# Kernel optimization log

Hardware: AMD Instinct MI355X
Metric: run time of the kernel (lower is better)

The kernel has to match this reference:

```python
import jax, jax.numpy as jnp
import numpy as np

N_NODES = 50000
N_EDGES = 600000
N_FEAT = 64
D = 128
N_GRAPHS = 1024
N_LAYERS = 4


def setup_inputs() -> dict:
    key = jax.random.key(0)
    ks = jax.random.split(key, 16)
    x = jax.random.normal(ks[0], (N_NODES, N_FEAT), dtype=jnp.float32)
    edge_index = jax.random.randint(ks[1], (2, N_EDGES), 0, N_NODES, dtype=jnp.int64)
    batch_index = jnp.sort(jax.random.randint(ks[2], (N_NODES,), 0, N_GRAPHS, dtype=jnp.int64))
    def lin(k, fan_in, fan_out):
        s = 1.0 / np.sqrt(fan_in)
        kw, kb = jax.random.split(k)
        w = jax.random.uniform(kw, (fan_in, fan_out), minval=-s, maxval=s, dtype=jnp.float32)
        b = jax.random.uniform(kb, (fan_out,), minval=-s, maxval=s, dtype=jnp.float32)
        return w, b
    w0, b0 = lin(ks[3], N_FEAT, D)
    w1, b1 = lin(ks[4], D, D)
    w2, b2 = lin(ks[5], D, D)
    w3, b3 = lin(ks[6], D, D)
    wp, bp = lin(ks[7], D, D)
    return {"x": x, "edge_index": edge_index, "batch_index": batch_index,
            "w0": w0, "b0": b0, "w1": w1, "b1": b1, "w2": w2, "b2": b2,
            "w3": w3, "b3": b3, "wp": wp, "bp": bp}


def _gin_layer(x, src, dst, w, b):
    # GINConv with eps=0: MLP(x_i + sum_{j in N(i)} x_j); MLP = Linear -> ReLU
    agg = jax.ops.segment_sum(x[src], dst, num_segments=N_NODES)
    return jax.nn.relu((x + agg) @ w + b)


def reference(x, edge_index, batch_index, w0, b0, w1, b1, w2, b2, w3, b3, wp, bp):
    src, dst = edge_index[0], edge_index[1]
    # first layer changes width 64 -> 128; agg happens in input width
    agg0 = jax.ops.segment_sum(x[src], dst, num_segments=N_NODES)
    h = jax.nn.relu((x + agg0) @ w0 + b0)
    for w, b in ((w1, b1), (w2, b2), (w3, b3)):
        h = _gin_layer(h, src, dst, w, b)
    # global mean pool per graph
    sums = jax.ops.segment_sum(h, batch_index, num_segments=N_GRAPHS)
    counts = jax.ops.segment_sum(jnp.ones((N_NODES,), dtype=h.dtype), batch_index, num_segments=N_GRAPHS)
    pooled = sums / jnp.maximum(counts, 1.0)[:, None]
    # post_mp: Linear -> ReLU (dropout identity at inference)
    return jax.nn.relu(pooled @ wp + bp)
```

## Files before the change

### kernel.cpp

```cpp
#include <hip/hip_runtime.h>
#include <hip/hip_fp16.h>


#define N_NODES  50000
#define N_EDGES  600000
#define N_FEAT   64
#define DIM      128
#define N_GRAPHS 1024
#define NC       7
#define CSH      13
#define TOT2     (N_NODES * NC)
#define SCH      2048
#define NBLK     ((TOT2 + SCH - 1) / SCH)
#define TPB      256
#define GT32     ((N_NODES + 31) / 32)

typedef _Float16 f16x8 __attribute__((ext_vector_type(8)));
typedef float    f32x4 __attribute__((ext_vector_type(4)));

#define CNTZ2 (TOT2 / 4)
#define XWORK (N_NODES * N_FEAT / 4)
#define CONV_TOTAL (XWORK + N_FEAT * DIM + 3 * DIM * DIM)
#define FILL_TOTAL (N_EDGES + CONV_TOTAL)

__global__ __launch_bounds__(TPB) void zero_k(int* __restrict__ cnt2) {
  int i = blockIdx.x * TPB + threadIdx.x;
  if (i < CNTZ2)
    *reinterpret_cast<int4*>(cnt2 + i * 4) = make_int4(0, 0, 0, 0);
}

__global__ __launch_bounds__(TPB) void hist_k(
    const int* __restrict__ src, const int* __restrict__ dst,
    int* __restrict__ cnt2, int* __restrict__ rank) {
  int e = blockIdx.x * TPB + threadIdx.x;
  if (e >= N_EDGES) return;
  int key = dst[e] * NC + (src[e] >> CSH);
  rank[e] = atomicAdd(&cnt2[key], 1);
}

__global__ __launch_bounds__(TPB) void scan_part_k(
    const int* __restrict__ cnt2, int* __restrict__ part) {
  __shared__ int ws[4];
  int t = threadIdx.x, b = blockIdx.x;
  int base = b * SCH + t * 8;
  int s = 0;
  if (base < TOT2) {
    int4 a = *reinterpret_cast<const int4*>(cnt2 + base);
    int4 c = *reinterpret_cast<const int4*>(cnt2 + base + 4);
    s = a.x + a.y + a.z + a.w + c.x + c.y + c.z + c.w;
  }
  for (int off = 32; off; off >>= 1) s += __shfl_down(s, off, 64);
  int lane = t & 63, wv = t >> 6;
  if (lane == 0) ws[wv] = s;
  __syncthreads();
  if (t == 0) part[b] = ws[0] + ws[1] + ws[2] + ws[3];
}

__global__ __launch_bounds__(TPB) void scan_write_k(
    const int* __restrict__ cnt2, const int* __restrict__ part,
    int* __restrict__ row_ptr2) {
  __shared__ int pscan[TPB];
  __shared__ int wsum[4];
  int t = threadIdx.x, b = blockIdx.x;
  int lane = t & 63, wv = t >> 6;
  int base = b * SCH + t * 8;

  pscan[t] = (t < NBLK) ? part[t] : 0;
  __syncthreads();
  for (int off = 1; off < TPB; off <<= 1) {
    int v = (t >= off) ? pscan[t - off] : 0;
    __syncthreads();
    pscan[t] += v;
    __syncthreads();
  }
  int blk_off = (b > 0) ? pscan[b - 1] : 0;

  int v[8] = {0,0,0,0,0,0,0,0};
  if (base < TOT2) {
    int4 a = *reinterpret_cast<const int4*>(cnt2 + base);
    int4 c = *reinterpret_cast<const int4*>(cnt2 + base + 4);
    v[0]=a.x; v[1]=a.y; v[2]=a.z; v[3]=a.w;
    v[4]=c.x; v[5]=c.y; v[6]=c.z; v[7]=c.w;
  }
  int ls = 0;
#pragma unroll
  for (int i = 0; i < 8; ++i) ls += v[i];
  int incl = ls;
  for (int off = 1; off < 64; off <<= 1) {
    int u = __shfl_up(incl, off, 64);
    if (lane >= off) incl += u;
  }
  if (lane == 63) wsum[wv] = incl;
  __syncthreads();
  int woff = 0;
  for (int w = 0; w < wv; ++w) woff += wsum[w];
  int run = blk_off + woff + (incl - ls);
  if (base < TOT2) {
    int rp[8];
#pragma unroll
    for (int i = 0; i < 8; ++i) { rp[i] = run; run += v[i]; }
    *reinterpret_cast<int4*>(row_ptr2 + base) = make_int4(rp[0], rp[1], rp[2], rp[3]);
    *reinterpret_cast<int4*>(row_ptr2 + base + 4) = make_int4(rp[4], rp[5], rp[6], rp[7]);
  }
  if (b == 0 && t == 0) row_ptr2[TOT2] = N_EDGES;
}

__global__ __launch_bounds__(TPB) void fill_k(
    const int* __restrict__ src, const int* __restrict__ dst,
    const int* __restrict__ row_ptr2, const int* __restrict__ rank,
    int* __restrict__ csr_src,
    const float* __restrict__ x, __half* __restrict__ xh,
    const float* __restrict__ w0, const float* __restrict__ w1,
    const float* __restrict__ w2, const float* __restrict__ w3,
    __half* __restrict__ Wt0, __half* __restrict__ Wt1,
    __half* __restrict__ Wt2, __half* __restrict__ Wt3) {
  int i = blockIdx.x * TPB + threadIdx.x;
  if (i < N_EDGES) {
    int s = src[i];
    int key = dst[i] * NC + (s >> CSH);
    csr_src[row_ptr2[key] + rank[i]] = s;
    return;
  }
  i -= N_EDGES;
  if (i < XWORK) {
    float4 v = *reinterpret_cast<const float4*>(x + (size_t)i * 4);
    union { __half2 h2[2]; uint2 u; } pk;
    pk.h2[0] = __floats2half2_rn(v.x, v.y);
    pk.h2[1] = __floats2half2_rn(v.z, v.w);
    *reinterpret_cast<uint2*>(xh + (size_t)i * 4) = pk.u;
    return;
  }
  int j = i - XWORK;
  if (j < N_FEAT * DIM) {
    int k = j >> 7, n = j & 127;
    Wt0[n * N_FEAT + k] = __float2half(w0[j]);
    return;
  }
  j -= N_FEAT * DIM;
  if (j >= 3 * DIM * DIM) return;
  int wsel = j / (DIM * DIM);
  int jj = j - wsel * (DIM * DIM);
  int k = jj >> 7, n = jj & 127;
  const float* W = (wsel == 0) ? w1 : (wsel == 1) ? w2 : w3;
  __half* Wt     = (wsel == 0) ? Wt1 : (wsel == 1) ? Wt2 : Wt3;
  Wt[n * DIM + k] = __float2half(W[jj]);
}

__global__ __launch_bounds__(TPB) void g64gg_k(
    const __half* __restrict__ xh, const int* __restrict__ row_ptr2,
    const int* __restrict__ csr_src,
    const __half* __restrict__ Wt0, const float* __restrict__ b0,
    const __half* __restrict__ Wt1, __half* __restrict__ y1) {
  __shared__ __align__(16) __half As[32][72];
  __shared__ __align__(16) __half Hs[32][136];
  const f16x8* xv = reinterpret_cast<const f16x8*>(xh);
  int tid = threadIdx.x;
  int row0 = blockIdx.x * 32;

  {
    int ns = tid >> 3, l = tid & 7;
    int node = row0 + ns;
    f16x8 o;
    if (node < N_NODES) {
      int beg = row_ptr2[node * NC];
      int end = row_ptr2[node * NC + NC];
      f16x8 self = xv[(size_t)node * 8 + l];
      float acc[8];
#pragma unroll
      for (int v = 0; v < 8; ++v) acc[v] = (float)self[v];
      int e = beg;
      for (; e + 3 < end; e += 4) {
        int s0 = csr_src[e+0], s1 = csr_src[e+1], s2 = csr_src[e+2], s3 = csr_src[e+3];
        f16x8 v0 = xv[(size_t)s0 * 8 + l];
        f16x8 v1 = xv[(size_t)s1 * 8 + l];
        f16x8 v2 = xv[(size_t)s2 * 8 + l];
        f16x8 v3 = xv[(size_t)s3 * 8 + l];
#pragma unroll
        for (int v = 0; v < 8; ++v)
          acc[v] += ((float)v0[v] + (float)v1[v]) + ((float)v2[v] + (float)v3[v]);
      }
      for (; e < end; ++e) {
        f16x8 v0 = xv[(size_t)csr_src[e] * 8 + l];
#pragma unroll
        for (int v = 0; v < 8; ++v) acc[v] += (float)v0[v];
      }
#pragma unroll
      for (int v = 0; v < 8; ++v) o[v] = (_Float16)acc[v];
    } else {
#pragma unroll
      for (int v = 0; v < 8; ++v) o[v] = (_Float16)0.f;
    }
    *reinterpret_cast<f16x8*>(&As[ns][l * 8]) = o;
  }
  __syncthreads();

  int w = tid >> 6, lane = tid & 63;
  int quad = lane >> 4, m = lane & 15;
  int col0 = w * 32;

  f32x4 accA[2][2];
#pragma unroll
  for (int mt = 0; mt < 2; ++mt)
#pragma unroll
    for (int nt = 0; nt < 2; ++nt) accA[mt][nt] = (f32x4){0.f,0.f,0.f,0.f};
#pragma unroll
  for (int kc = 0; kc < 2; ++kc) {
    f16x8 a0 = *reinterpret_cast<const f16x8*>(&As[m][kc*32 + quad*8]);
    f16x8 a1 = *reinterpret_cast<const f16x8*>(&As[16 + m][kc*32 + quad*8]);
#pragma unroll
    for (int nt = 0; nt < 2; ++nt) {
      f16x8 b = *reinterpret_cast<const f16x8*>(
          Wt0 + (size_t)(col0 + nt*16 + m) * N_FEAT + kc*32 + quad*8);
      accA[0][nt] = __builtin_amdgcn_mfma_f32_16x16x32_f16(a0, b, accA[0][nt], 0, 0, 0);
      accA[1][nt] = __builtin_amdgcn_mfma_f32_16x16x32_f16(a1, b, accA[1][nt], 0, 0, 0);
    }
  }
#pragma unroll
  for (int mt = 0; mt < 2; ++mt)
#pragma unroll
    for (int nt = 0; nt < 2; ++nt) {
      float bv = b0[col0 + nt*16 + m];
#pragma unroll
      for (int r = 0; r < 4; ++r)
        Hs[mt*16 + quad*4 + r][col0 + nt*16 + m] =
            __float2half(fmaxf(accA[mt][nt][r] + bv, 0.f));
    }
  __syncthreads();

  f32x4 accB[2][2];
#pragma unroll
  for (int mt = 0; mt < 2; ++mt)
#pragma unroll
    for (int nt = 0; nt < 2; ++nt) accB[mt][nt] = (f32x4){0.f,0.f,0.f,0.f};
#pragma unroll
  for (int kc = 0; kc < 4; ++kc) {
    f16x8 a0 = *reinterpret_cast<const f16x8*>(&Hs[m][kc*32 + quad*8]);
    f16x8 a1 = *reinterpret_cast<const f16x8*>(&Hs[16 + m][kc*32 + quad*8]);
#pragma unroll
    for (int nt = 0; nt < 2; ++nt) {
      f16x8 b = *reinterpret_cast<const f16x8*>(
          Wt1 + (size_t)(col0 + nt*16 + m) * DIM + kc*32 + quad*8);
      accB[0][nt] = __builtin_amdgcn_mfma_f32_16x16x32_f16(a0, b, accB[0][nt], 0, 0, 0);
      accB[1][nt] = __builtin_amdgcn_mfma_f32_16x16x32_f16(a1, b, accB[1][nt], 0, 0, 0);
    }
  }
  __syncthreads();
#pragma unroll
  for (int mt = 0; mt < 2; ++mt)
#pragma unroll
    for (int nt = 0; nt < 2; ++nt)
#pragma unroll
      for (int r = 0; r < 4; ++r)
        Hs[mt*16 + quad*4 + r][col0 + nt*16 + m] = __float2half(accB[mt][nt][r]);
  __syncthreads();
#pragma unroll
  for (int it = 0; it < 2; ++it) {
    int i = tid + it * TPB;
    int r = i >> 4, c = (i & 15) * 8;
    int row = row0 + r;
    if (row < N_NODES)
      *reinterpret_cast<f16x8*>(y1 + (size_t)row * DIM + c) =
          *reinterpret_cast<const f16x8*>(&Hs[r][c]);
  }
}

__global__ __launch_bounds__(TPB) void fgg_k(
    const __half* __restrict__ y, const int* __restrict__ row_ptr2,
    const int* __restrict__ csr_src, const float* __restrict__ bias,
    const __half* __restrict__ Wn, __half* __restrict__ yout) {
  __shared__ __align__(16) __half As[32][136];
  const f16x8* yv = reinterpret_cast<const f16x8*>(y);
  int tid = threadIdx.x;
  int row0 = blockIdx.x * 32;
  int g = tid >> 4, l = tid & 15;

#pragma unroll 1
  for (int p = 0; p < 2; ++p) {
    int node = row0 + p * 16 + g;
    if (node < N_NODES) {
      int beg = row_ptr2[node * NC];
      int end = row_ptr2[node * NC + NC];
      f16x8 self = yv[(size_t)node * 16 + l];
      float acc[8];
#pragma unroll
      for (int v = 0; v < 8; ++v) acc[v] = (float)self[v];
      int e = beg;
      for (; e + 3 < end; e += 4) {
        int s0 = csr_src[e+0], s1 = csr_src[e+1], s2 = csr_src[e+2], s3 = csr_src[e+3];
        f16x8 v0 = yv[(size_t)s0 * 16 + l];
        f16x8 v1 = yv[(size_t)s1 * 16 + l];
        f16x8 v2 = yv[(size_t)s2 * 16 + l];
        f16x8 v3 = yv[(size_t)s3 * 16 + l];
#pragma unroll
        for (int v = 0; v < 8; ++v)
          acc[v] += ((float)v0[v] + (float)v1[v]) + ((float)v2[v] + (float)v3[v]);
      }
      for (; e < end; ++e) {
        f16x8 v0 = yv[(size_t)csr_src[e] * 16 + l];
#pragma unroll
        for (int v = 0; v < 8; ++v) acc[v] += (float)v0[v];
      }
      float4 bb0 = *reinterpret_cast<const float4*>(bias + l * 8);
      float4 bb1 = *reinterpret_cast<const float4*>(bias + l * 8 + 4);
      float bb[8] = {bb0.x, bb0.y, bb0.z, bb0.w, bb1.x, bb1.y, bb1.z, bb1.w};
      f16x8 o;
#pragma unroll
      for (int v = 0; v < 8; ++v) o[v] = (_Float16)fmaxf(acc[v] + bb[v], 0.f);
      *reinterpret_cast<f16x8*>(&As[p * 16 + g][l * 8]) = o;
    }
  }
  __syncthreads();

  int w = tid >> 6, lane = tid & 63;
  int quad = lane >> 4, m = lane & 15;
  int col0 = w * 32;
  f32x4 acc2[2][2];
#pragma unroll
  for (int mt = 0; mt < 2; ++mt)
#pragma unroll
    for (int nt = 0; nt < 2; ++nt) acc2[mt][nt] = (f32x4){0.f,0.f,0.f,0.f};
#pragma unroll
  for (int kc = 0; kc < 4; ++kc) {
    f16x8 a0 = *reinterpret_cast<const f16x8*>(&As[m][kc*32 + quad*8]);
    f16x8 a1 = *reinterpret_cast<const f16x8*>(&As[16 + m][kc*32 + quad*8]);
#pragma unroll
    for (int nt = 0; nt < 2; ++nt) {
      f16x8 b = *reinterpret_cast<const f16x8*>(
          Wn + (size_t)(col0 + nt*16 + m) * DIM + kc*32 + quad*8);
      acc2[0][nt] = __builtin_amdgcn_mfma_f32_16x16x32_f16(a0, b, acc2[0][nt], 0, 0, 0);
      acc2[1][nt] = __builtin_amdgcn_mfma_f32_16x16x32_f16(a1, b, acc2[1][nt], 0, 0, 0);
    }
  }
  __syncthreads();
#pragma unroll
  for (int mt = 0; mt < 2; ++mt)
#pragma unroll
    for (int nt = 0; nt < 2; ++nt)
#pragma unroll
      for (int r = 0; r < 4; ++r)
        As[mt*16 + quad*4 + r][col0 + nt*16 + m] = __float2half(acc2[mt][nt][r]);
  __syncthreads();
#pragma unroll
  for (int it = 0; it < 2; ++it) {
    int i = tid + it * TPB;
    int r = i >> 4, c = (i & 15) * 8;
    int row = row0 + r;
    if (row < N_NODES)
      *reinterpret_cast<f16x8*>(yout + (size_t)row * DIM + c) =
          *reinterpret_cast<const f16x8*>(&As[r][c]);
  }
}

template<int F, bool BR>
__global__ __launch_bounds__(TPB) void gather_k(
    const __half* __restrict__ y, const int* __restrict__ row_ptr2,
    const int* __restrict__ csr_src, const float* __restrict__ bias,
    __half* __restrict__ hout) {
  constexpr int CH = F / 8;
  const f16x8* yv = reinterpret_cast<const f16x8*>(y);
  int gid  = blockIdx.x * TPB + threadIdx.x;
  int node = gid / CH;
  int l    = gid % CH;
  if (node >= N_NODES) return;
  int beg = row_ptr2[node * NC];
  int end = row_ptr2[node * NC + NC];

  f16x8 self = yv[(size_t)node * CH + l];
  float acc[8];
#pragma unroll
  for (int v = 0; v < 8; ++v) acc[v] = (float)self[v];

  int e = beg;
  for (; e + 3 < end; e += 4) {
    int s0 = csr_src[e+0], s1 = csr_src[e+1], s2 = csr_src[e+2], s3 = csr_src[e+3];
    f16x8 v0 = yv[(size_t)s0 * CH + l];
    f16x8 v1 = yv[(size_t)s1 * CH + l];
    f16x8 v2 = yv[(size_t)s2 * CH + l];
    f16x8 v3 = yv[(size_t)s3 * CH + l];
#pragma unroll
    for (int v = 0; v < 8; ++v)
      acc[v] += ((float)v0[v] + (float)v1[v]) + ((float)v2[v] + (float)v3[v]);
  }
  for (; e < end; ++e) {
    f16x8 v0 = yv[(size_t)csr_src[e] * CH + l];
#pragma unroll
    for (int v = 0; v < 8; ++v) acc[v] += (float)v0[v];
  }

  f16x8 o;
  if (BR) {
    float4 b0 = *reinterpret_cast<const float4*>(bias + l * 8);
    float4 b1 = *reinterpret_cast<const float4*>(bias + l * 8 + 4);
    float bb[8] = {b0.x, b0.y, b0.z, b0.w, b1.x, b1.y, b1.z, b1.w};
#pragma unroll
    for (int v = 0; v < 8; ++v) o[v] = (_Float16)fmaxf(acc[v] + bb[v], 0.f);
  } else {
#pragma unroll
    for (int v = 0; v < 8; ++v) o[v] = (_Float16)acc[v];
  }
  reinterpret_cast<f16x8*>(hout)[(size_t)node * CH + l] = o;
}

__global__ __launch_bounds__(128) void pool_post_k(
    const __half* __restrict__ h, const int* __restrict__ batch,
    const float* __restrict__ W, const float* __restrict__ bias,
    float* __restrict__ out) {
  __shared__ float xs[DIM];
  int g = blockIdx.x;
  int col = threadIdx.x;
  int lo = 0, hi = N_NODES;
  while (lo < hi) { int mid = (lo + hi) >> 1; if (batch[mid] < g) lo = mid + 1; else hi = mid; }
  int beg = lo;
  hi = N_NODES;
  while (lo < hi) { int mid = (lo + hi) >> 1; if (batch[mid] < g + 1) lo = mid + 1; else hi = mid; }
  int end = lo;

  float acc = 0.f;
  for (int n = beg; n < end; ++n) acc += __half2float(h[(size_t)n * DIM + col]);
  float cnt = fmaxf((float)(end - beg), 1.0f);
  xs[col] = acc / cnt;
  __syncthreads();
  float o = bias[col];
  for (int k = 0; k < DIM; ++k)
    o = fmaf(xs[k], W[(size_t)k * DIM + col], o);
  out[(size_t)g * DIM + col] = fmaxf(o, 0.f);
}

extern "C" void kernel_launch(void* const* d_in, const int* in_sizes, int n_in,
                              void* d_out, int out_size, void* d_ws, size_t ws_size,
                              hipStream_t stream) {
  const float* x    = (const float*)d_in[0];
  const int*   ei   = (const int*)d_in[1];
  const int*   batch= (const int*)d_in[2];
  const float* w0 = (const float*)d_in[3];  const float* b0 = (const float*)d_in[4];
  const float* w1 = (const float*)d_in[5];  const float* b1 = (const float*)d_in[6];
  const float* w2 = (const float*)d_in[7];  const float* b2 = (const float*)d_in[8];
  const float* w3 = (const float*)d_in[9];  const float* b3 = (const float*)d_in[10];
  const float* wp = (const float*)d_in[11]; const float* bp = (const float*)d_in[12];
  float* out = (float*)d_out;

  const int* src = ei;
  const int* dst = ei + N_EDGES;

  __half* xh = (__half*)d_ws;
  __half* yA = xh + (size_t)N_NODES * N_FEAT;
  __half* yB = yA + (size_t)N_NODES * DIM;
  __half* h  = yB + (size_t)N_NODES * DIM;
  __half* Wt0 = h + (size_t)N_NODES * DIM;
  __half* Wt1 = Wt0 + N_FEAT * DIM;
  __half* Wt2 = Wt1 + DIM * DIM;
  __half* Wt3 = Wt2 + DIM * DIM;
  int* cnt2     = (int*)(Wt3 + DIM * DIM);
  int* rank     = cnt2 + TOT2;
  int* part     = rank + N_EDGES;
  int* row_ptr2 = part + 256;
  int* csr_src  = row_ptr2 + (TOT2 + 1);

  zero_k<<<(CNTZ2 + TPB - 1) / TPB, TPB, 0, stream>>>(cnt2);
  hist_k<<<(N_EDGES + TPB - 1) / TPB, TPB, 0, stream>>>(src, dst, cnt2, rank);
  scan_part_k <<<NBLK, TPB, 0, stream>>>(cnt2, part);
  scan_write_k<<<NBLK, TPB, 0, stream>>>(cnt2, part, row_ptr2);
  fill_k<<<(FILL_TOTAL + TPB - 1) / TPB, TPB, 0, stream>>>(
      src, dst, row_ptr2, rank, csr_src,
      x, xh, w0, w1, w2, w3, Wt0, Wt1, Wt2, Wt3);

  g64gg_k<<<GT32, TPB, 0, stream>>>(xh, row_ptr2, csr_src, Wt0, b0, Wt1, yA);

  fgg_k<<<GT32, TPB, 0, stream>>>(yA, row_ptr2, csr_src, b1, Wt2, yB);
  fgg_k<<<GT32, TPB, 0, stream>>>(yB, row_ptr2, csr_src, b2, Wt3, yA);

  gather_k<DIM, true><<<(N_NODES * 16 + TPB - 1) / TPB, TPB, 0, stream>>>(
      yA, row_ptr2, csr_src, b3, h);

  pool_post_k<<<N_GRAPHS, 128, 0, stream>>>(h, batch, wp, bp, out);
}
```

Measured before the change: 256.7 us.

## Fuse final-layer gather with per-graph mean-pool partial sums

The last aggregation + bias + ReLU is fused into a per-graph kernel that accumulates pooled partial sums directly, split 4 ways per graph, instead of writing the full node feature matrix and re-reading it in the pool kernel. The post kernel then sums four partials and applies the final linear layer. This removes a 50000x128 fp16 write and read plus the slow serial per-column pooling loop. The cost is fewer threads working on the gather and possible load imbalance across graphs of different sizes.

```diff
diff --git a/kernel.cpp b/kernel.cpp
--- a/kernel.cpp
+++ b/kernel.cpp
@@ -14,6 +14,7 @@
 #define NBLK     ((TOT2 + SCH - 1) / SCH)
 #define TPB      256
 #define GT32     ((N_NODES + 31) / 32)
+#define GSPLIT   4
 
 typedef _Float16 f16x8 __attribute__((ext_vector_type(8)));
 typedef float    f32x4 __attribute__((ext_vector_type(4)));
@@ -351,58 +352,72 @@
   }
 }
 
-template<int F, bool BR>
-__global__ __launch_bounds__(TPB) void gather_k(
+__global__ __launch_bounds__(TPB) void gpp_k(
     const __half* __restrict__ y, const int* __restrict__ row_ptr2,
     const int* __restrict__ csr_src, const float* __restrict__ bias,
-    __half* __restrict__ hout) {
-  constexpr int CH = F / 8;
+    const int* __restrict__ batch, float* __restrict__ partial) {
+  __shared__ float red[16][DIM];
   const f16x8* yv = reinterpret_cast<const f16x8*>(y);
-  int gid  = blockIdx.x * TPB + threadIdx.x;
-  int node = gid / CH;
-  int l    = gid % CH;
-  if (node >= N_NODES) return;
-  int beg = row_ptr2[node * NC];
-  int end = row_ptr2[node * NC + NC];
-
-  f16x8 self = yv[(size_t)node * CH + l];
-  float acc[8];
-#pragma unroll
-  for (int v = 0; v < 8; ++v) acc[v] = (float)self[v];
-
-  int e = beg;
-  for (; e + 3 < end; e += 4) {
-    int s0 = csr_src[e+0], s1 = csr_src[e+1], s2 = csr_src[e+2], s3 = csr_src[e+3];
-    f16x8 v0 = yv[(size_t)s0 * CH + l];
-    f16x8 v1 = yv[(size_t)s1 * CH + l];
-    f16x8 v2 = yv[(size_t)s2 * CH + l];
-    f16x8 v3 = yv[(size_t)s3 * CH + l];
-#pragma unroll
-    for (int v = 0; v < 8; ++v)
-      acc[v] += ((float)v0[v] + (float)v1[v]) + ((float)v2[v] + (float)v3[v]);
-  }
-  for (; e < end; ++e) {
-    f16x8 v0 = yv[(size_t)csr_src[e] * CH + l];
-#pragma unroll
-    for (int v = 0; v < 8; ++v) acc[v] += (float)v0[v];
-  }
-
-  f16x8 o;
-  if (BR) {
-    float4 b0 = *reinterpret_cast<const float4*>(bias + l * 8);
-    float4 b1 = *reinterpret_cast<const float4*>(bias + l * 8 + 4);
-    float bb[8] = {b0.x, b0.y, b0.z, b0.w, b1.x, b1.y, b1.z, b1.w};
-#pragma unroll
-    for (int v = 0; v < 8; ++v) o[v] = (_Float16)fmaxf(acc[v] + bb[v], 0.f);
-  } else {
-#pragma unroll
-    for (int v = 0; v < 8; ++v) o[v] = (_Float16)acc[v];
-  }
-  reinterpret_cast<f16x8*>(hout)[(size_t)node * CH + l] = o;
-}
-
-__global__ __launch_bounds__(128) void pool_post_k(
-    const __half* __restrict__ h, const int* __restrict__ batch,
+  int g = blockIdx.x >> 2, p = blockIdx.x & 3;
+  int t = threadIdx.x;
+  int s = t >> 4, l = t & 15;
+
+  int lo = 0, hi = N_NODES;
+  while (lo < hi) { int mid = (lo + hi) >> 1; if (batch[mid] < g) lo = mid + 1; else hi = mid; }
+  int beg = lo;
+  hi = N_NODES;
+  while (lo < hi) { int mid = (lo + hi) >> 1; if (batch[mid] < g + 1) lo = mid + 1; else hi = mid; }
+  int end = lo;
+
+  float4 bb0 = *reinterpret_cast<const float4*>(bias + l * 8);
+  float4 bb1 = *reinterpret_cast<const float4*>(bias + l * 8 + 4);
+  float bb[8] = {bb0.x, bb0.y, bb0.z, bb0.w, bb1.x, bb1.y, bb1.z, bb1.w};
+
+  float pacc[8];
+#pragma unroll
+  for (int v = 0; v < 8; ++v) pacc[v] = 0.f;
+
+  for (int i = p + GSPLIT * s; beg + i < end; i += GSPLIT * 16) {
+    int node = beg + i;
+    int eb = row_ptr2[node * NC];
+    int ee = row_ptr2[node * NC + NC];
+    f16x8 self = yv[(size_t)node * 16 + l];
+    float acc[8];
+#pragma unroll
+    for (int v = 0; v < 8; ++v) acc[v] = (float)self[v];
+    int e = eb;
+    for (; e + 3 < ee; e += 4) {
+      int s0 = csr_src[e+0], s1 = csr_src[e+1], s2 = csr_src[e+2], s3 = csr_src[e+3];
+      f16x8 v0 = yv[(size_t)s0 * 16 + l];
+      f16x8 v1 = yv[(size_t)s1 * 16 + l];
+      f16x8 v2 = yv[(size_t)s2 * 16 + l];
+      f16x8 v3 = yv[(size_t)s3 * 16 + l];
+#pragma unroll
+      for (int v = 0; v < 8; ++v)
+        acc[v] += ((float)v0[v] + (float)v1[v]) + ((float)v2[v] + (float)v3[v]);
+    }
+    for (; e < ee; ++e) {
+      f16x8 v0 = yv[(size_t)csr_src[e] * 16 + l];
+#pragma unroll
+      for (int v = 0; v < 8; ++v) acc[v] += (float)v0[v];
+    }
+#pragma unroll
+    for (int v = 0; v < 8; ++v) pacc[v] += fmaxf(acc[v] + bb[v], 0.f);
+  }
+
+#pragma unroll
+  for (int v = 0; v < 8; ++v) red[s][l * 8 + v] = pacc[v];
+  __syncthreads();
+  if (t < DIM) {
+    float sum = 0.f;
+#pragma unroll
+    for (int ss = 0; ss < 16; ++ss) sum += red[ss][t];
+    partial[((size_t)g * GSPLIT + p) * DIM + t] = sum;
+  }
+}
+
+__global__ __launch_bounds__(128) void post_k(
+    const float* __restrict__ partial, const int* __restrict__ batch,
     const float* __restrict__ W, const float* __restrict__ bias,
     float* __restrict__ out) {
   __shared__ float xs[DIM];
@@ -415,10 +430,12 @@
   while (lo < hi) { int mid = (lo + hi) >> 1; if (batch[mid] < g + 1) lo = mid + 1; else hi = mid; }
   int end = lo;
 
-  float acc = 0.f;
-  for (int n = beg; n < end; ++n) acc += __half2float(h[(size_t)n * DIM + col]);
   float cnt = fmaxf((float)(end - beg), 1.0f);
-  xs[col] = acc / cnt;
+  float sum = 0.f;
+#pragma unroll
+  for (int p = 0; p < GSPLIT; ++p)
+    sum += partial[((size_t)g * GSPLIT + p) * DIM + col];
+  xs[col] = sum / cnt;
   __syncthreads();
   float o = bias[col];
   for (int k = 0; k < DIM; ++k)
@@ -445,12 +462,12 @@
   __half* xh = (__half*)d_ws;
   __half* yA = xh + (size_t)N_NODES * N_FEAT;
   __half* yB = yA + (size_t)N_NODES * DIM;
-  __half* h  = yB + (size_t)N_NODES * DIM;
-  __half* Wt0 = h + (size_t)N_NODES * DIM;
+  __half* Wt0 = yB + (size_t)N_NODES * DIM;
   __half* Wt1 = Wt0 + N_FEAT * DIM;
   __half* Wt2 = Wt1 + DIM * DIM;
   __half* Wt3 = Wt2 + DIM * DIM;
-  int* cnt2     = (int*)(Wt3 + DIM * DIM);
+  float* partial = (float*)(Wt3 + DIM * DIM);
+  int* cnt2     = (int*)(partial + (size_t)N_GRAPHS * GSPLIT * DIM);
   int* rank     = cnt2 + TOT2;
   int* part     = rank + N_EDGES;
   int* row_ptr2 = part + 256;
@@ -469,8 +486,7 @@
   fgg_k<<<GT32, TPB, 0, stream>>>(yA, row_ptr2, csr_src, b1, Wt2, yB);
   fgg_k<<<GT32, TPB, 0, stream>>>(yB, row_ptr2, csr_src, b2, Wt3, yA);
 
-  gather_k<DIM, true><<<(N_NODES * 16 + TPB - 1) / TPB, TPB, 0, stream>>>(
-      yA, row_ptr2, csr_src, b3, h);
-
-  pool_post_k<<<N_GRAPHS, 128, 0, stream>>>(h, batch, wp, bp, out);
-}
+  gpp_k<<<N_GRAPHS * GSPLIT, TPB, 0, stream>>>(
+      yA, row_ptr2, csr_src, b3, batch, partial);
+  post_k<<<N_GRAPHS, 128, 0, stream>>>(partial, batch, wp, bp, out);
+}
```

New measurement: 256.4 us (median of 2 runs). No clear change (-0.1%).
